# Performance work log

Measured on AMD Instinct MI355X. Metric: run time of the kernel, lower is better.

Reference implementation:

```python
import jax, jax.numpy as jnp
import numpy as np

B, H, S, D = 4, 16, 2048, 128

def setup_inputs() -> dict:
    key = jax.random.key(0)
    kk, kq, kv = jax.random.split(key, 3)
    k = jax.random.normal(kk, (B, H, S, D), dtype=jnp.float32)
    q = jax.random.normal(kq, (B, H, S, D), dtype=jnp.float32)
    v = jax.random.normal(kv, (B, H, S, D), dtype=jnp.float32)
    # causal mask: True = masked out (strictly upper triangle)
    mask = jnp.triu(jnp.ones((S, S), dtype=bool), k=1)
    return {"k": k, "q": q, "v": v, "mask": mask}

def reference(k, q, v, mask):
    d_k = k.shape[-1]
    # scores: [B, H, S, S]
    scores = jnp.einsum("bhqd,bhkd->bhqk", q, k) / jnp.sqrt(jnp.asarray(d_k, q.dtype))
    scores = jnp.where(mask, -jnp.inf, scores)
    # numerically stable softmax over last dim (matches manual max/exp/sum)
    p = jax.nn.softmax(scores, axis=-1)
    return jnp.einsum("bhqk,bhkd->bhqd", p, v)
```

## Files before the change

kernel.cpp:

```cpp
#include <hip/hip_runtime.h>
#include <hip/hip_bf16.h>
#include <math.h>

#define BATCH 4
#define HEADS 16
#define SEQ   2048
#define DIM   128
#define BHN   (BATCH*HEADS)

#define BQ 128
#define WQ 32
#define KT 32
#define NXB (SEQ/BQ)

typedef short bf16x8 __attribute__((ext_vector_type(8)));
typedef float f32x4  __attribute__((ext_vector_type(4)));

static __device__ __forceinline__ unsigned short f2bf(float f) {
    union { float f; unsigned u; } x; x.f = f;
    unsigned r = x.u + 0x7FFF + ((x.u >> 16) & 1);
    return (unsigned short)(r >> 16);
}

static __device__ __forceinline__ void async_cp16(const unsigned short* g, unsigned short* l) {
    __builtin_amdgcn_global_load_lds(
        (const __attribute__((address_space(1))) unsigned int*)g,
        (__attribute__((address_space(3))) unsigned int*)l,
        16, 0, 0);
}

__global__ __launch_bounds__(256) void cvt_kv(
    const float* __restrict__ k, const float* __restrict__ v,
    unsigned short* __restrict__ kb, unsigned short* __restrict__ vt) {
    __shared__ unsigned short T[DIM][72];
    const int bh = blockIdx.y;
    const int s0 = blockIdx.x * 64;
    const int t  = threadIdx.x;
    const long rbase = ((long)bh * SEQ + s0) * DIM;

    #pragma unroll
    for (int u = 0; u < 2; ++u) {
        long e = rbase + (long)(t + u * 256) * 16;
        const float* src = k + e;
        unsigned short* dst = kb + e;
        #pragma unroll
        for (int h = 0; h < 2; ++h) {
            float4 a0 = *(const float4*)(src + h * 8);
            float4 a1 = *(const float4*)(src + h * 8 + 4);
            union { uint4 u4; unsigned short s[8]; } p;
            p.s[0]=f2bf(a0.x); p.s[1]=f2bf(a0.y); p.s[2]=f2bf(a0.z); p.s[3]=f2bf(a0.w);
            p.s[4]=f2bf(a1.x); p.s[5]=f2bf(a1.y); p.s[6]=f2bf(a1.z); p.s[7]=f2bf(a1.w);
            *(uint4*)(dst + h * 8) = p.u4;
        }
    }
    {
        const int r = t >> 2, i = t & 3;
        const float* src = v + rbase + (long)r * DIM + i * 32;
        #pragma unroll
        for (int j = 0; j < 8; ++j) {
            float4 x = *(const float4*)(src + j * 4);
            const int d = i * 32 + j * 4;
            T[d + 0][r] = f2bf(x.x); T[d + 1][r] = f2bf(x.y);
            T[d + 2][r] = f2bf(x.z); T[d + 3][r] = f2bf(x.w);
        }
    }
    __syncthreads();
    {
        const int d = t >> 1, h = t & 1;
        unsigned short* dst = vt + ((long)bh * DIM + d) * SEQ + s0 + h * 32;
        #pragma unroll
        for (int m = 0; m < 4; ++m)
            *(uint4*)(dst + m * 8) = *(const uint4*)&T[d][h * 32 + m * 8];
    }
}

__global__ __launch_bounds__(256, 2) void attn_fwd(
    const float* __restrict__ qg,
    const unsigned short* __restrict__ kb,
    const unsigned short* __restrict__ vtg,
    float* __restrict__ out) {

    __shared__ unsigned short Kt[2][KT][DIM];
    __shared__ unsigned short Vt[2][DIM][KT];
    __shared__ unsigned short Pl[4][16][KT + 8];

    const int tid  = threadIdx.x;
    const int w    = tid >> 6;
    const int lane = tid & 63;
    const int quad = lane >> 4;
    const int ql   = lane & 15;

    const int flat = blockIdx.x;
    const int xcd  = flat & 7;
    const int slot = flat >> 3;
    const int bh   = (xcd << 3) | (slot & 7);
    const int shi  = slot >> 3;
    const int xb   = (shi < 4) ? (15 - shi)
                   : (shi < 8) ? (shi - 4)
                   : (shi < 12) ? shi
                   : (19 - shi);
    const int qb0 = xb * BQ;
    const int qw0 = qb0 + w * WQ;

    const long base = (long)bh * SEQ * DIM;
    const float scale = 0.08838834764831845f;

    bf16x8 qf[2][4];
    #pragma unroll
    for (int mb = 0; mb < 2; ++mb) {
        const float* qr = qg + base + (long)(qw0 + mb * 16 + ql) * DIM;
        #pragma unroll
        for (int c = 0; c < 4; ++c) {
            const float* p = qr + c * 32 + quad * 8;
            float4 x = *(const float4*)(p);
            float4 y = *(const float4*)(p + 4);
            union { bf16x8 v; unsigned short s[8]; } u;
            u.s[0]=f2bf(x.x*scale); u.s[1]=f2bf(x.y*scale);
            u.s[2]=f2bf(x.z*scale); u.s[3]=f2bf(x.w*scale);
            u.s[4]=f2bf(y.x*scale); u.s[5]=f2bf(y.y*scale);
            u.s[6]=f2bf(y.z*scale); u.s[7]=f2bf(y.w*scale);
            qf[mb][c] = u.v;
        }
    }

    f32x4 acc[2][8];
    #pragma unroll
    for (int mb = 0; mb < 2; ++mb)
        #pragma unroll
        for (int n = 0; n < 8; ++n)
            acc[mb][n] = (f32x4){0.f, 0.f, 0.f, 0.f};

    float m_[2] = {-INFINITY, -INFINITY};
    float l_[2] = {0.f, 0.f};

    auto stage = [&](int buf, int k0) {
        #pragma unroll
        for (int i = 0; i < 2; ++i) {
            const int idx = tid + i * 256;
            const int r   = idx >> 4;
            const int chg = (idx & 15) ^ (r & 15);
            async_cp16(kb + base + (long)(k0 + r) * DIM + chg * 8,
                       &Kt[buf][0][0] + ((tid >> 6) * 64 + i * 256) * 8);
            const int d   = idx >> 2;
            const int cvg = (idx & 3) ^ ((d >> 1) & 3);
            async_cp16(vtg + base + (long)d * SEQ + k0 + cvg * 8,
                       &Vt[buf][0][0] + ((tid >> 6) * 64 + i * 256) * 8);
        }
    };

    const int ntile = (qb0 + BQ) / KT;

    stage(0, 0);

    for (int t = 0; t < ntile; ++t) {
        const int buf = t & 1;
        const int k0  = t * KT;
        __syncthreads();

        if (t + 1 < ntile) stage(buf ^ 1, k0 + KT);

        const bool active = (k0 < qw0 + WQ);
        if (active) {
            f32x4 sacc[2][2];
            #pragma unroll
            for (int mb = 0; mb < 2; ++mb)
                #pragma unroll
                for (int kk = 0; kk < 2; ++kk)
                    sacc[mb][kk] = (f32x4){0.f, 0.f, 0.f, 0.f};
            #pragma unroll
            for (int c = 0; c < 4; ++c) {
                const int sw = ((c * 4 + quad) ^ ql) * 8;
                bf16x8 kf0 = *(const bf16x8*)&Kt[buf][ql]     [sw];
                bf16x8 kf1 = *(const bf16x8*)&Kt[buf][16 + ql][sw];
                #pragma unroll
                for (int mb = 0; mb < 2; ++mb) {
                    sacc[mb][0] = __builtin_amdgcn_mfma_f32_16x16x32_bf16(kf0, qf[mb][c], sacc[mb][0], 0, 0, 0);
                    sacc[mb][1] = __builtin_amdgcn_mfma_f32_16x16x32_bf16(kf1, qf[mb][c], sacc[mb][1], 0, 0, 0);
                }
            }

            bf16x8 vf[8];
            #pragma unroll
            for (int n = 0; n < 8; ++n)
                vf[n] = *(const bf16x8*)&Vt[buf][n * 16 + ql][(quad ^ ((ql >> 1) & 3)) * 8];

            #pragma unroll
            for (int mb = 0; mb < 2; ++mb) {
                const int qrow   = qw0 + mb * 16 + ql;
                const bool needm = (k0 + KT - 1 > qw0 + mb * 16);
                float s[2][4];
                float tmax = -INFINITY;
                #pragma unroll
                for (int kk = 0; kk < 2; ++kk)
                    #pragma unroll
                    for (int r = 0; r < 4; ++r) {
                        float sv = sacc[mb][kk][r];
                        if (needm) {
                            int kg = k0 + kk * 16 + quad * 4 + r;
                            sv = (kg <= qrow) ? sv : -INFINITY;
                        }
                        s[kk][r] = sv;
                        tmax = fmaxf(tmax, sv);
                    }
                tmax = fmaxf(tmax, __shfl_xor(tmax, 16));
                tmax = fmaxf(tmax, __shfl_xor(tmax, 32));
                float mnew  = fmaxf(m_[mb], tmax);
                float alpha = __expf(m_[mb] - mnew);
                float rsum = 0.f;
                #pragma unroll
                for (int kk = 0; kk < 2; ++kk)
                    #pragma unroll
                    for (int r = 0; r < 4; ++r) {
                        float p = __expf(s[kk][r] - mnew);
                        s[kk][r] = p;
                        rsum += p;
                    }
                rsum += __shfl_xor(rsum, 16);
                rsum += __shfl_xor(rsum, 32);
                l_[mb] = l_[mb] * alpha + rsum;
                m_[mb] = mnew;

                #pragma unroll
                for (int kk = 0; kk < 2; ++kk) {
                    union { uint2 u; unsigned short h[4]; } pu;
                    #pragma unroll
                    for (int r = 0; r < 4; ++r) pu.h[r] = f2bf(s[kk][r]);
                    *(uint2*)&Pl[w][ql][kk * 16 + quad * 4] = pu.u;
                }

                #pragma unroll
                for (int r = 0; r < 4; ++r) {
                    float ar = __shfl(alpha, quad * 4 + r);
                    #pragma unroll
                    for (int n = 0; n < 8; ++n) acc[mb][n][r] *= ar;
                }

                bf16x8 pf = *(const bf16x8*)&Pl[w][ql][quad * 8];
                #pragma unroll
                for (int n = 0; n < 8; ++n)
                    acc[mb][n] = __builtin_amdgcn_mfma_f32_16x16x32_bf16(pf, vf[n], acc[mb][n], 0, 0, 0);
            }
        }
    }

    #pragma unroll
    for (int mb = 0; mb < 2; ++mb) {
        #pragma unroll
        for (int r = 0; r < 4; ++r) {
            float lr = __shfl(l_[mb], quad * 4 + r);
            float il = 1.0f / lr;
            long orow = base + (long)(qw0 + mb * 16 + quad * 4 + r) * DIM;
            #pragma unroll
            for (int n = 0; n < 8; ++n)
                out[orow + n * 16 + ql] = acc[mb][n][r] * il;
        }
    }
}

extern "C" void kernel_launch(void* const* d_in, const int* in_sizes, int n_in,
                              void* d_out, int out_size, void* d_ws, size_t ws_size,
                              hipStream_t stream) {
    const float* k = (const float*)d_in[0];
    const float* q = (const float*)d_in[1];
    const float* v = (const float*)d_in[2];
    float* o = (float*)d_out;

    unsigned short* kb = (unsigned short*)d_ws;
    unsigned short* vt = kb + (size_t)BHN * SEQ * DIM;

    cvt_kv<<<dim3(SEQ / 64, BHN), dim3(256), 0, stream>>>(k, v, kb, vt);

    attn_fwd<<<dim3(NXB * BHN), dim3(256), 0, stream>>>(q, kb, vt, o);
}
```

Before: 357.8 us.

## Use exp2 softmax with lazy rescale and split P staging per row block

Folds log2(e) into the Q scale so the softmax uses native exp2 in place of __expf. It skips the running-max update and the accumulator rescale when the whole wavefront's tile max stays within a threshold of the current max. The scalar bf16 conversions are replaced with paired bf16x2 conversions. P is staged in separate LDS buffers for each row block so both loads happen before the PV MFMAs. The lazy rescale adds a wave vote and a branch, and lets unnormalized P values grow up to 2^8, which bf16 and fp32 can hold.

```diff
diff --git a/kernel.cpp b/kernel.cpp
--- a/kernel.cpp
+++ b/kernel.cpp
@@ -82,7 +82,7 @@
 
     __shared__ unsigned short Kt[2][KT][DIM];
     __shared__ unsigned short Vt[2][DIM][KT];
-    __shared__ unsigned short Pl[4][16][KT + 8];
+    __shared__ unsigned short Pl[4][2][16][KT + 8];
 
     const int tid  = threadIdx.x;
     const int w    = tid >> 6;
@@ -103,7 +103,7 @@
     const int qw0 = qb0 + w * WQ;
 
     const long base = (long)bh * SEQ * DIM;
-    const float scale = 0.08838834764831845f;
+    const float scale = 0.08838834764831845f * 1.4426950408889634f;
 
     bf16x8 qf[2][4];
     #pragma unroll
@@ -184,6 +184,8 @@
             for (int n = 0; n < 8; ++n)
                 vf[n] = *(const bf16x8*)&Vt[buf][n * 16 + ql][(quad ^ ((ql >> 1) & 3)) * 8];
 
+            float alpha_[2];
+            bool  resc_[2];
             #pragma unroll
             for (int mb = 0; mb < 2; ++mb) {
                 const int qrow   = qw0 + mb * 16 + ql;
@@ -204,38 +206,51 @@
                     }
                 tmax = fmaxf(tmax, __shfl_xor(tmax, 16));
                 tmax = fmaxf(tmax, __shfl_xor(tmax, 32));
-                float mnew  = fmaxf(m_[mb], tmax);
-                float alpha = __expf(m_[mb] - mnew);
+
+                const bool skip = __all(tmax <= m_[mb] + 8.0f);
+                const float mnew = skip ? m_[mb] : fmaxf(m_[mb], tmax);
+
                 float rsum = 0.f;
                 #pragma unroll
-                for (int kk = 0; kk < 2; ++kk)
+                for (int kk = 0; kk < 2; ++kk) {
+                    float p0 = __builtin_amdgcn_exp2f(s[kk][0] - mnew);
+                    float p1 = __builtin_amdgcn_exp2f(s[kk][1] - mnew);
+                    float p2 = __builtin_amdgcn_exp2f(s[kk][2] - mnew);
+                    float p3 = __builtin_amdgcn_exp2f(s[kk][3] - mnew);
+                    rsum += (p0 + p1) + (p2 + p3);
+                    union { uint2 u; __hip_bfloat162 h[2]; } pu;
+                    pu.h[0] = __float22bfloat162_rn(float2{p0, p1});
+                    pu.h[1] = __float22bfloat162_rn(float2{p2, p3});
+                    *(uint2*)&Pl[w][mb][ql][kk * 16 + quad * 4] = pu.u;
+                }
+                rsum += __shfl_xor(rsum, 16);
+                rsum += __shfl_xor(rsum, 32);
+
+                if (skip) {
+                    l_[mb] += rsum;
+                    alpha_[mb] = 1.f; resc_[mb] = false;
+                } else {
+                    const float al = __builtin_amdgcn_exp2f(m_[mb] - mnew);
+                    l_[mb] = l_[mb] * al + rsum;
+                    m_[mb] = mnew;
+                    alpha_[mb] = al; resc_[mb] = true;
+                }
+            }
+
+            bf16x8 pf0 = *(const bf16x8*)&Pl[w][0][ql][quad * 8];
+            bf16x8 pf1 = *(const bf16x8*)&Pl[w][1][ql][quad * 8];
+
+            #pragma unroll
+            for (int mb = 0; mb < 2; ++mb) {
+                if (resc_[mb]) {
                     #pragma unroll
                     for (int r = 0; r < 4; ++r) {
-                        float p = __expf(s[kk][r] - mnew);
-                        s[kk][r] = p;
-                        rsum += p;
+                        float ar = __shfl(alpha_[mb], quad * 4 + r);
+                        #pragma unroll
+                        for (int n = 0; n < 8; ++n) acc[mb][n][r] *= ar;
                     }
-                rsum += __shfl_xor(rsum, 16);
-                rsum += __shfl_xor(rsum, 32);
-                l_[mb] = l_[mb] * alpha + rsum;
-                m_[mb] = mnew;
-
-                #pragma unroll
-                for (int kk = 0; kk < 2; ++kk) {
-                    union { uint2 u; unsigned short h[4]; } pu;
-                    #pragma unroll
-                    for (int r = 0; r < 4; ++r) pu.h[r] = f2bf(s[kk][r]);
-                    *(uint2*)&Pl[w][ql][kk * 16 + quad * 4] = pu.u;
-                }
-
-                #pragma unroll
-                for (int r = 0; r < 4; ++r) {
-                    float ar = __shfl(alpha, quad * 4 + r);
-                    #pragma unroll
-                    for (int n = 0; n < 8; ++n) acc[mb][n][r] *= ar;
-                }
-
-                bf16x8 pf = *(const bf16x8*)&Pl[w][ql][quad * 8];
+                }
+                const bf16x8 pf = mb ? pf1 : pf0;
                 #pragma unroll
                 for (int n = 0; n < 8; ++n)
                     acc[mb][n] = __builtin_amdgcn_mfma_f32_16x16x32_bf16(pf, vf[n], acc[mb][n], 0, 0, 0);
```

Measured after the change: 352.4 us. About the same (-1.5%).
